# Kernel optimization log

Hardware: AMD Instinct MI355X
Metric: run time of the kernel (lower is better)

Reference implementation:

```python
import jax, jax.numpy as jnp
import numpy as np

N, E, IN, H, C = 50000, 400000, 128, 8, 32
NEG_SLOPE = 0.2


def setup_inputs() -> dict:
    key = jax.random.key(0)
    ks = jax.random.split(key, 8)
    s = 0.1
    return {
        "x": jax.random.normal(ks[0], (N, IN), jnp.float32),
        "edge_index": jax.random.randint(ks[1], (2, E), 0, N, dtype=jnp.int32),
        "edge_attr": jax.random.normal(ks[2], (E, 1), jnp.float32),
        "batch": jnp.zeros((N,), jnp.int32),
        "W_l": jax.random.normal(ks[3], (H * C, IN), jnp.float32) * s,
        "W_r": jax.random.normal(ks[4], (H * C, IN), jnp.float32) * s,
        "W_e": jax.random.normal(ks[5], (H * C, 1), jnp.float32) * s,
        "att": jax.random.normal(ks[6], (H, C), jnp.float32) * s,
        "bias": jnp.zeros((C,), jnp.float32),
        "W_proj": jax.random.normal(ks[7], (C, IN), jnp.float32) * s,
    }


def reference(x, edge_index, edge_attr, batch, W_l, W_r, W_e, att, bias, W_proj):
    n = x.shape[0]
    # --- add self loops (PyG default), edge_attr fill = 'mean' ---
    loop = jnp.arange(n, dtype=edge_index.dtype)
    ei = jnp.concatenate([edge_index, jnp.stack([loop, loop])], axis=1)  # [2, E+N]
    loop_attr = jnp.broadcast_to(edge_attr.mean(axis=0), (n, edge_attr.shape[1]))
    ea = jnp.concatenate([edge_attr, loop_attr], axis=0)                 # [E+N, 1]
    src, dst = ei[0], ei[1]

    # --- node transforms (GATv2: separate lin_l / lin_r) ---
    x_l = (x @ W_l.T).reshape(n, H, C)   # source-side features
    x_r = (x @ W_r.T).reshape(n, H, C)   # destination-side features
    e_feat = (ea @ W_e.T).reshape(-1, H, C)  # [E+N, H, C] edge fusion

    # --- GATv2 attention logits ---
    m = x_l[src] + x_r[dst] + e_feat                 # [E+N, H, C]
    m = jax.nn.leaky_relu(m, NEG_SLOPE)
    alpha = jnp.einsum("ehc,hc->eh", m, att)         # [E+N, H]

    # --- softmax over edges grouped by destination node ---
    amax = jax.ops.segment_max(alpha, dst, num_segments=n)  # [N, H]
    aexp = jnp.exp(alpha - amax[dst])
    denom = jax.ops.segment_sum(aexp, dst, num_segments=n)
    alpha = aexp / denom[dst]                        # [E+N, H]

    # --- weighted aggregation of source messages ---
    out = jax.ops.segment_sum(x_l[src] * alpha[:, :, None], dst, num_segments=n)  # [N, H, C]
    out = out.mean(axis=1) + bias                    # concat=False -> head mean, [N, C]

    # --- relu + projected residual ---
    x_new = jax.nn.relu(out) + x @ W_proj.T          # [N, C]
    return (x_new, alpha)
```

## Files before the change

### kernel.cpp

```cpp
#include <hip/hip_runtime.h>
#include <math.h>

#define N_NODES 50000
#define N_EDGES 400000
#define EN_TOT  450000
#define IN_DIM  128
#define H_HEADS 8
#define C_CH    32
#define HC      256
#define NEG_SLOPE 0.2f
#define MAXDEG 64

typedef __attribute__((ext_vector_type(8))) short bf16x8;
typedef __attribute__((ext_vector_type(4))) float f32x4;

#define OFF_XLB   0
#define OFF_XRB   (OFF_XLB + N_NODES * 128)
#define OFF_PROJ  (OFF_XRB + N_NODES * 128)
#define OFF_AEXP  (OFF_PROJ + N_NODES * C_CH)
#define OFF_WCAT  (OFF_AEXP + EN_TOT * H_HEADS)
#define OFF_PART  (OFF_WCAT + 34816)
#define OFF_MEAN  (OFF_PART + 1024)
#define OFF_PAD   (OFF_MEAN + 1)
#define OFF_CSR4  (OFF_PAD + 3)
#define OFF_DEG   (OFF_CSR4 + EN_TOT * 4)
#define OFF_OFFS  (OFF_DEG + N_NODES)
#define OFF_CUR   (OFF_OFFS + N_NODES + 1)
#define OFF_BSUM  (OFF_CUR + N_NODES)

#define SCAN_B 196

__device__ __forceinline__ unsigned f2bf(float f) {
    unsigned u = __float_as_uint(f);
    u += 0x7fffu + ((u >> 16) & 1u);
    return u >> 16;
}
__device__ __forceinline__ float bflo(unsigned u) { return __uint_as_float(u << 16); }
__device__ __forceinline__ float bfhi(unsigned u) { return __uint_as_float(u & 0xffff0000u); }

#define WCHUNKS 8704
__global__ __launch_bounds__(256) void pre_kernel(
    const float* __restrict__ Wl, const float* __restrict__ Wr, const float* __restrict__ Wproj,
    unsigned short* __restrict__ wcat,
    const int* __restrict__ ei, const float* __restrict__ ea,
    int* __restrict__ deg, float* __restrict__ part)
{
    __shared__ float sd[256];
    const int t = threadIdx.x;
    const int g = blockIdx.x * 256 + t;

    if (g < WCHUNKS) {
        int j = (g * 8) >> 7, k = (g * 8) & 127;
        const float* src = (j < 256 ? Wl + (size_t)j * 128
                                    : (j < 512 ? Wr + (size_t)(j - 256) * 128
                                               : Wproj + (size_t)(j - 512) * 128)) + k;
        float4 a = ((const float4*)src)[0];
        float4 b = ((const float4*)src)[1];
        uint4 o;
        o.x = f2bf(a.x) | (f2bf(a.y) << 16);
        o.y = f2bf(a.z) | (f2bf(a.w) << 16);
        o.z = f2bf(b.x) | (f2bf(b.y) << 16);
        o.w = f2bf(b.z) | (f2bf(b.w) << 16);
        ((uint4*)wcat)[g] = o;
    }

    float s = 0.f;
    for (int i = g; i < N_EDGES; i += 1024 * 256) s += ea[i];
    for (int i = g; i < EN_TOT; i += 1024 * 256) {
        int d = (i < N_EDGES) ? ei[N_EDGES + i] : (i - N_EDGES);
        atomicAdd(&deg[d], 1);
    }
    sd[t] = s; __syncthreads();
    for (int w = 128; w > 0; w >>= 1) { if (t < w) sd[t] += sd[t + w]; __syncthreads(); }
    if (t == 0) part[blockIdx.x] = sd[0];
}

__global__ __launch_bounds__(256) void scan_part_kernel(const int* __restrict__ deg,
                                                        int* __restrict__ bsum) {
    __shared__ int sd[256];
    int t = threadIdx.x;
    int i = blockIdx.x * 256 + t;
    int v = (i < N_NODES) ? deg[i] : 0;
    sd[t] = v; __syncthreads();
    for (int w = 128; w > 0; w >>= 1) { if (t < w) sd[t] += sd[t + w]; __syncthreads(); }
    if (t == 0) bsum[blockIdx.x] = sd[0];
}

__global__ __launch_bounds__(256) void mid_kernel(int* __restrict__ bsum,
                                                  const float* __restrict__ part,
                                                  float* __restrict__ mean_out) {
    __shared__ int sd[256];
    __shared__ float sf[256];
    int t = threadIdx.x;
    float s = part[t] + part[t + 256] + part[t + 512] + part[t + 768];
    sf[t] = s;
    int v = (t < SCAN_B) ? bsum[t] : 0;
    sd[t] = v; __syncthreads();
    for (int w = 128; w > 0; w >>= 1) { if (t < w) sf[t] += sf[t + w]; __syncthreads(); }
    if (t == 0) mean_out[0] = sf[0] / (float)N_EDGES;
    #pragma unroll
    for (int ofs = 1; ofs < 256; ofs <<= 1) {
        int u = (t >= ofs) ? sd[t - ofs] : 0;
        __syncthreads();
        sd[t] += u;
        __syncthreads();
    }
    if (t < SCAN_B) bsum[t] = sd[t] - v;
}

__global__ __launch_bounds__(256) void scan_final_kernel(
    const int* __restrict__ deg, const int* __restrict__ bsum,
    int* __restrict__ offs, int* __restrict__ cur) {
    __shared__ int sd[256];
    int t = threadIdx.x;
    int i = blockIdx.x * 256 + t;
    int v = (i < N_NODES) ? deg[i] : 0;
    sd[t] = v; __syncthreads();
    #pragma unroll
    for (int ofs = 1; ofs < 256; ofs <<= 1) {
        int u = (t >= ofs) ? sd[t - ofs] : 0;
        __syncthreads();
        sd[t] += u;
        __syncthreads();
    }
    int excl = bsum[blockIdx.x] + sd[t] - v;
    if (i < N_NODES) { offs[i] = excl; cur[i] = excl; }
    if (i == N_NODES - 1) offs[N_NODES] = excl + v;
}

__global__ __launch_bounds__(256) void scatter_kernel(
    const int* __restrict__ ei, const float* __restrict__ edge_attr,
    const float* __restrict__ mean_attr, int* __restrict__ cur,
    int4* __restrict__ csr4)
{
    int e = blockIdx.x * 256 + threadIdx.x;
    if (e >= EN_TOT) return;
    int s, d; float eav;
    if (e < N_EDGES) { s = ei[e]; d = ei[N_EDGES + e]; eav = edge_attr[e]; }
    else { s = e - N_EDGES; d = s; eav = mean_attr[0]; }
    int pos = atomicAdd(&cur[d], 1);
    csr4[pos] = make_int4(s, e, __float_as_int(eav), 0);
}

#define GM 128
#define GN 64

__global__ __launch_bounds__(256) void gemm_mfma_kernel(
    const float* __restrict__ x, const unsigned short* __restrict__ wcat,
    unsigned short* __restrict__ xlb, unsigned short* __restrict__ xrb,
    float* __restrict__ proj)
{
    __shared__ unsigned short As[GM * 128];
    __shared__ unsigned short Bs[GN * 128];
    const int t = threadIdx.x;
    const int m0 = blockIdx.x * GM;
    const int n0 = blockIdx.y * GN;

    #pragma unroll
    for (int cc = 0; cc < 8; ++cc) {
        int c = t + cc * 256;
        int r = c >> 4;
        int k0 = (c & 15) * 8;
        int row = m0 + r;
        uint4 o = make_uint4(0, 0, 0, 0);
        if (row < N_NODES) {
            const float* p = x + (size_t)row * IN_DIM + k0;
            float4 a = ((const float4*)p)[0];
            float4 b = ((const float4*)p)[1];
            o.x = f2bf(a.x) | (f2bf(a.y) << 16);
            o.y = f2bf(a.z) | (f2bf(a.w) << 16);
            o.z = f2bf(b.x) | (f2bf(b.y) << 16);
            o.w = f2bf(b.z) | (f2bf(b.w) << 16);
        }
        int byte = (r * 256 + k0 * 2) ^ ((r & 7) << 4);
        *((uint4*)((char*)As + byte)) = o;
    }
    #pragma unroll
    for (int cc = 0; cc < 4; ++cc) {
        int c = t + cc * 256;
        int r = c >> 4;
        int k0 = (c & 15) * 8;
        int j = n0 + r;
        uint4 v = make_uint4(0, 0, 0, 0);
        if (j < 544) v = *((const uint4*)(wcat + (size_t)j * 128 + k0));
        int byte = (r * 256 + k0 * 2) ^ ((r & 7) << 4);
        *((uint4*)((char*)Bs + byte)) = v;
    }
    __syncthreads();

    const int wid = t >> 6, lane = t & 63;
    const int wr = wid >> 1, wc = wid & 1;
    const int lrow = lane & 15;
    const int kgrp = (lane >> 4) * 8;

    f32x4 acc[4][2] = {};
    #pragma unroll
    for (int kk = 0; kk < 4; ++kk) {
        bf16x8 a[4], b[2];
        #pragma unroll
        for (int fm = 0; fm < 4; ++fm) {
            int r = wr * 64 + fm * 16 + lrow;
            int byte = (r * 256 + (kk * 32 + kgrp) * 2) ^ ((r & 7) << 4);
            a[fm] = *((const bf16x8*)((const char*)As + byte));
        }
        #pragma unroll
        for (int fn = 0; fn < 2; ++fn) {
            int r = wc * 32 + fn * 16 + lrow;
            int byte = (r * 256 + (kk * 32 + kgrp) * 2) ^ ((r & 7) << 4);
            b[fn] = *((const bf16x8*)((const char*)Bs + byte));
        }
        #pragma unroll
        for (int fm = 0; fm < 4; ++fm)
            #pragma unroll
            for (int fn = 0; fn < 2; ++fn)
                acc[fm][fn] = __builtin_amdgcn_mfma_f32_16x16x32_bf16(a[fm], b[fn], acc[fm][fn], 0, 0, 0);
    }

    const int crow0 = (lane >> 4) * 4;
    const int ccol = lane & 15;
    #pragma unroll
    for (int fm = 0; fm < 4; ++fm) {
        #pragma unroll
        for (int fn = 0; fn < 2; ++fn) {
            #pragma unroll
            for (int r = 0; r < 4; ++r) {
                int row = m0 + wr * 64 + fm * 16 + crow0 + r;
                int col = n0 + wc * 32 + fn * 16 + ccol;
                if (row >= N_NODES) continue;
                float v = acc[fm][fn][r];
                if (col < 256)      xlb[(size_t)row * HC + col] = (unsigned short)f2bf(v);
                else if (col < 512) xrb[(size_t)row * HC + (col - 256)] = (unsigned short)f2bf(v);
                else if (col < 544) proj[(size_t)row * C_CH + (col - 512)] = v;
            }
        }
    }
}

__global__ __launch_bounds__(256) void node_agg_kernel(
    const int* __restrict__ offs, const int4* __restrict__ csr4,
    const float* __restrict__ We, const float* __restrict__ att,
    const unsigned short* __restrict__ xlb, const unsigned short* __restrict__ xrb,
    const float* __restrict__ proj, const float* __restrict__ bias,
    float* __restrict__ aexp_ovf, float* __restrict__ alpha_out, float* __restrict__ xnew)
{
    __shared__ float s_aexp[4][MAXDEG][H_HEADS];
    __shared__ int   s_eid[4][MAXDEG];
    const int w = threadIdx.x >> 6;
    const int l = threadIdx.x & 63;
    const int d = blockIdx.x * 4 + w;
    if (d >= N_NODES) return;
    const int half = l >> 5;
    const int sl = l & 31;

    const float4 we0 = ((const float4*)We)[sl * 2];
    const float4 we1 = ((const float4*)We)[sl * 2 + 1];
    const float4 at0 = ((const float4*)att)[sl * 2];
    const float4 at1 = ((const float4*)att)[sl * 2 + 1];
    const float wev[8] = {we0.x, we0.y, we0.z, we0.w, we1.x, we1.y, we1.z, we1.w};
    const float atv[8] = {at0.x, at0.y, at0.z, at0.w, at1.x, at1.y, at1.z, at1.w};

    const uint4 vru = ((const uint4*)(xrb + (size_t)d * HC))[sl];
    float vr[8];
    vr[0] = bflo(vru.x); vr[1] = bfhi(vru.x); vr[2] = bflo(vru.y); vr[3] = bfhi(vru.y);
    vr[4] = bflo(vru.z); vr[5] = bfhi(vru.z); vr[6] = bflo(vru.w); vr[7] = bfhi(vru.w);

    const int beg = offs[d];
    const int end = offs[d + 1];

    float acc[8] = {0.f, 0.f, 0.f, 0.f, 0.f, 0.f, 0.f, 0.f};
    float den = 0.f;

    int i = beg;
    int4 c0 = make_int4(0, 0, 0, 0);
    uint4 vl0 = make_uint4(0, 0, 0, 0);
    if (i + half < end) {
        c0 = csr4[i + half];
        vl0 = ((const uint4*)(xlb + (size_t)c0.x * HC))[sl];
    }
    while (i < end) {
        const int ni = i + 2;
        int4 c1 = make_int4(0, 0, 0, 0);
        uint4 vl1 = make_uint4(0, 0, 0, 0);
        if (ni + half < end) {
            c1 = csr4[ni + half];
            vl1 = ((const uint4*)(xlb + (size_t)c1.x * HC))[sl];
        }

        const float ea = __int_as_float(c0.z);
        float xv[8];
        xv[0] = bflo(vl0.x); xv[1] = bfhi(vl0.x); xv[2] = bflo(vl0.y); xv[3] = bfhi(vl0.y);
        xv[4] = bflo(vl0.z); xv[5] = bfhi(vl0.z); xv[6] = bflo(vl0.w); xv[7] = bfhi(vl0.w);

        float tt = 0.f;
        #pragma unroll
        for (int j = 0; j < 8; ++j) {
            float m = xv[j] + vr[j] + ea * wev[j];
            m = fmaxf(m, NEG_SLOPE * m);
            tt += m * atv[j];
        }
        tt += __shfl_xor(tt, 1);
        tt += __shfl_xor(tt, 2);
        float aex = __expf(tt);
        const bool valid = (i + half) < end;
        aex = valid ? aex : 0.f;
        const int li = i + half - beg;
        if (valid && (sl & 3) == 0) {
            if (li < MAXDEG) s_aexp[w][li][sl >> 2] = aex;
            else             aexp_ovf[(size_t)c0.y * H_HEADS + (sl >> 2)] = aex;
        }
        if (valid && sl == 0 && li < MAXDEG) s_eid[w][li] = c0.y;
        #pragma unroll
        for (int j = 0; j < 8; ++j) acc[j] += aex * xv[j];
        den += aex;

        c0 = c1; vl0 = vl1; i = ni;
    }

    den += __shfl_xor(den, 32);
    #pragma unroll
    for (int j = 0; j < 8; ++j) acc[j] += __shfl_xor(acc[j], 32);

    const float den_h = __shfl(den, ((l & 7) << 2));
    const float rden = 1.f / den_h;
    for (int b = beg; b < end; b += 8) {
        const int idx = b + (l >> 3);
        if (idx < end) {
            const int li = idx - beg;
            int e; float ax;
            if (li < MAXDEG) { e = s_eid[w][li]; ax = s_aexp[w][li][l & 7]; }
            else { e = csr4[idx].y; ax = aexp_ovf[(size_t)e * H_HEADS + (l & 7)]; }
            alpha_out[(size_t)e * H_HEADS + (l & 7)] = ax * rden;
        }
    }

    const float inv = 1.f / den;
    #pragma unroll
    for (int j = 0; j < 8; ++j) acc[j] *= inv;
    #pragma unroll
    for (int mask = 4; mask <= 16; mask <<= 1)
        #pragma unroll
        for (int j = 0; j < 8; ++j) acc[j] += __shfl_xor(acc[j], mask);
    if (half == 0 && sl < 4) {
        const float4 bi0 = ((const float4*)bias)[sl * 2];
        const float4 bi1 = ((const float4*)bias)[sl * 2 + 1];
        const float4 pr0 = ((const float4*)(proj + (size_t)d * C_CH))[sl * 2];
        const float4 pr1 = ((const float4*)(proj + (size_t)d * C_CH))[sl * 2 + 1];
        float4 r0, r1;
        r0.x = fmaxf(acc[0] * 0.125f + bi0.x, 0.f) + pr0.x;
        r0.y = fmaxf(acc[1] * 0.125f + bi0.y, 0.f) + pr0.y;
        r0.z = fmaxf(acc[2] * 0.125f + bi0.z, 0.f) + pr0.z;
        r0.w = fmaxf(acc[3] * 0.125f + bi0.w, 0.f) + pr0.w;
        r1.x = fmaxf(acc[4] * 0.125f + bi1.x, 0.f) + pr1.x;
        r1.y = fmaxf(acc[5] * 0.125f + bi1.y, 0.f) + pr1.y;
        r1.z = fmaxf(acc[6] * 0.125f + bi1.z, 0.f) + pr1.z;
        r1.w = fmaxf(acc[7] * 0.125f + bi1.w, 0.f) + pr1.w;
        ((float4*)(xnew + (size_t)d * C_CH))[sl * 2] = r0;
        ((float4*)(xnew + (size_t)d * C_CH))[sl * 2 + 1] = r1;
    }
}

extern "C" void kernel_launch(void* const* d_in, const int* in_sizes, int n_in,
                              void* d_out, int out_size, void* d_ws, size_t ws_size,
                              hipStream_t stream) {
    const float* x         = (const float*)d_in[0];
    const int*   ei        = (const int*)d_in[1];
    const float* edge_attr = (const float*)d_in[2];
    const float* Wl        = (const float*)d_in[4];
    const float* Wr        = (const float*)d_in[5];
    const float* We        = (const float*)d_in[6];
    const float* att       = (const float*)d_in[7];
    const float* bias      = (const float*)d_in[8];
    const float* Wproj     = (const float*)d_in[9];

    float* ws    = (float*)d_ws;
    unsigned short* xlb  = (unsigned short*)(ws + OFF_XLB);
    unsigned short* xrb  = (unsigned short*)(ws + OFF_XRB);
    float* proj  = ws + OFF_PROJ;
    float* aexp  = ws + OFF_AEXP;
    unsigned short* wcat = (unsigned short*)(ws + OFF_WCAT);
    float* part  = ws + OFF_PART;
    float* meanp = ws + OFF_MEAN;
    int4*  csr4  = (int4*)(ws + OFF_CSR4);
    int*   deg   = (int*)(ws + OFF_DEG);
    int*   offs  = (int*)(ws + OFF_OFFS);
    int*   cur   = (int*)(ws + OFF_CUR);
    int*   bsum  = (int*)(ws + OFF_BSUM);

    float* out_xnew  = (float*)d_out;
    float* out_alpha = (float*)d_out + (size_t)N_NODES * C_CH;

    hipMemsetAsync(deg, 0, N_NODES * sizeof(int), stream);

    pre_kernel<<<1024, 256, 0, stream>>>(Wl, Wr, Wproj, wcat, ei, edge_attr, deg, part);

    scan_part_kernel<<<SCAN_B, 256, 0, stream>>>(deg, bsum);
    mid_kernel<<<1, 256, 0, stream>>>(bsum, part, meanp);
    scan_final_kernel<<<SCAN_B, 256, 0, stream>>>(deg, bsum, offs, cur);

    scatter_kernel<<<(EN_TOT + 255) / 256, 256, 0, stream>>>(ei, edge_attr, meanp, cur, csr4);

    dim3 ggrid((N_NODES + GM - 1) / GM, (544 + GN - 1) / GN);
    gemm_mfma_kernel<<<ggrid, 256, 0, stream>>>(x, wcat, xlb, xrb, proj);

    node_agg_kernel<<<(N_NODES + 3) / 4, 256, 0, stream>>>(offs, csr4, We, att, xlb, xrb,
                                                           proj, bias, aexp, out_alpha, out_xnew);
}
```

Measured before the change: 175.6 us.

## Pack CSR entries to 8 bytes and vectorize attention math with packed floats

The CSR record shrinks from int4 to int2: the source index (which fits in 16 bits) and a bf16-rounded edge attribute share one word, and the edge id sits in the other. This halves CSR write and read traffic in the scatter and aggregation kernels. The aggregation loop now uses float2 vector types so the compiler can emit packed FP32 ops. Leaky ReLU is rewritten as 0.6*m + 0.4*|m| with log2e folded into the weights, so the exponential becomes exp2f. The costs are bf16 precision loss on edge_attr and a dependence on node indices staying below 65536.

```diff
diff --git a/kernel.cpp b/kernel.cpp
--- a/kernel.cpp
+++ b/kernel.cpp
@@ -13,6 +13,7 @@
 
 typedef __attribute__((ext_vector_type(8))) short bf16x8;
 typedef __attribute__((ext_vector_type(4))) float f32x4;
+typedef __attribute__((ext_vector_type(2))) float f32x2;
 
 #define OFF_XLB   0
 #define OFF_XRB   (OFF_XLB + N_NODES * 128)
@@ -22,13 +23,14 @@
 #define OFF_PART  (OFF_WCAT + 34816)
 #define OFF_MEAN  (OFF_PART + 1024)
 #define OFF_PAD   (OFF_MEAN + 1)
-#define OFF_CSR4  (OFF_PAD + 3)
-#define OFF_DEG   (OFF_CSR4 + EN_TOT * 4)
+#define OFF_CSR2  (OFF_PAD + 3)
+#define OFF_DEG   (OFF_CSR2 + EN_TOT * 2)
 #define OFF_OFFS  (OFF_DEG + N_NODES)
 #define OFF_CUR   (OFF_OFFS + N_NODES + 1)
 #define OFF_BSUM  (OFF_CUR + N_NODES)
 
 #define SCAN_B 196
+#define LOG2E 1.4426950408889634f
 
 __device__ __forceinline__ unsigned f2bf(float f) {
     unsigned u = __float_as_uint(f);
@@ -37,6 +39,7 @@
 }
 __device__ __forceinline__ float bflo(unsigned u) { return __uint_as_float(u << 16); }
 __device__ __forceinline__ float bfhi(unsigned u) { return __uint_as_float(u & 0xffff0000u); }
+__device__ __forceinline__ f32x2 unpk(unsigned u) { f32x2 r; r.x = bflo(u); r.y = bfhi(u); return r; }
 
 #define WCHUNKS 8704
 __global__ __launch_bounds__(256) void pre_kernel(
@@ -131,7 +134,7 @@
 __global__ __launch_bounds__(256) void scatter_kernel(
     const int* __restrict__ ei, const float* __restrict__ edge_attr,
     const float* __restrict__ mean_attr, int* __restrict__ cur,
-    int4* __restrict__ csr4)
+    int2* __restrict__ csr2)
 {
     int e = blockIdx.x * 256 + threadIdx.x;
     if (e >= EN_TOT) return;
@@ -139,7 +142,7 @@
     if (e < N_EDGES) { s = ei[e]; d = ei[N_EDGES + e]; eav = edge_attr[e]; }
     else { s = e - N_EDGES; d = s; eav = mean_attr[0]; }
     int pos = atomicAdd(&cur[d], 1);
-    csr4[pos] = make_int4(s, e, __float_as_int(eav), 0);
+    csr2[pos] = make_int2(s | (int)(f2bf(eav) << 16), e);
 }
 
 #define GM 128
@@ -237,7 +240,7 @@
 }
 
 __global__ __launch_bounds__(256) void node_agg_kernel(
-    const int* __restrict__ offs, const int4* __restrict__ csr4,
+    const int* __restrict__ offs, const int2* __restrict__ csr2,
     const float* __restrict__ We, const float* __restrict__ att,
     const unsigned short* __restrict__ xlb, const unsigned short* __restrict__ xrb,
     const float* __restrict__ proj, const float* __restrict__ bias,
@@ -256,51 +259,59 @@
     const float4 we1 = ((const float4*)We)[sl * 2 + 1];
     const float4 at0 = ((const float4*)att)[sl * 2];
     const float4 at1 = ((const float4*)att)[sl * 2 + 1];
-    const float wev[8] = {we0.x, we0.y, we0.z, we0.w, we1.x, we1.y, we1.z, we1.w};
-    const float atv[8] = {at0.x, at0.y, at0.z, at0.w, at1.x, at1.y, at1.z, at1.w};
+    f32x2 we2[4], a06[4], a04[4];
+    we2[0].x = we0.x; we2[0].y = we0.y; we2[1].x = we0.z; we2[1].y = we0.w;
+    we2[2].x = we1.x; we2[2].y = we1.y; we2[3].x = we1.z; we2[3].y = we1.w;
+    a06[0].x = at0.x; a06[0].y = at0.y; a06[1].x = at0.z; a06[1].y = at0.w;
+    a06[2].x = at1.x; a06[2].y = at1.y; a06[3].x = at1.z; a06[3].y = at1.w;
+    #pragma unroll
+    for (int j = 0; j < 4; ++j) {
+        a04[j] = a06[j] * (0.4f * LOG2E);
+        a06[j] = a06[j] * (0.6f * LOG2E);
+    }
 
     const uint4 vru = ((const uint4*)(xrb + (size_t)d * HC))[sl];
-    float vr[8];
-    vr[0] = bflo(vru.x); vr[1] = bfhi(vru.x); vr[2] = bflo(vru.y); vr[3] = bfhi(vru.y);
-    vr[4] = bflo(vru.z); vr[5] = bfhi(vru.z); vr[6] = bflo(vru.w); vr[7] = bfhi(vru.w);
+    f32x2 vr2[4] = {unpk(vru.x), unpk(vru.y), unpk(vru.z), unpk(vru.w)};
 
     const int beg = offs[d];
     const int end = offs[d + 1];
 
-    float acc[8] = {0.f, 0.f, 0.f, 0.f, 0.f, 0.f, 0.f, 0.f};
+    f32x2 acc2[4] = {};
     float den = 0.f;
 
     int i = beg;
-    int4 c0 = make_int4(0, 0, 0, 0);
+    int2 c0 = make_int2(0, 0);
     uint4 vl0 = make_uint4(0, 0, 0, 0);
     if (i + half < end) {
-        c0 = csr4[i + half];
-        vl0 = ((const uint4*)(xlb + (size_t)c0.x * HC))[sl];
+        c0 = csr2[i + half];
+        vl0 = ((const uint4*)(xlb + (size_t)(c0.x & 0xffff) * HC))[sl];
     }
     while (i < end) {
         const int ni = i + 2;
-        int4 c1 = make_int4(0, 0, 0, 0);
+        int2 c1 = make_int2(0, 0);
         uint4 vl1 = make_uint4(0, 0, 0, 0);
         if (ni + half < end) {
-            c1 = csr4[ni + half];
-            vl1 = ((const uint4*)(xlb + (size_t)c1.x * HC))[sl];
-        }
-
-        const float ea = __int_as_float(c0.z);
-        float xv[8];
-        xv[0] = bflo(vl0.x); xv[1] = bfhi(vl0.x); xv[2] = bflo(vl0.y); xv[3] = bfhi(vl0.y);
-        xv[4] = bflo(vl0.z); xv[5] = bfhi(vl0.z); xv[6] = bflo(vl0.w); xv[7] = bfhi(vl0.w);
-
-        float tt = 0.f;
-        #pragma unroll
-        for (int j = 0; j < 8; ++j) {
-            float m = xv[j] + vr[j] + ea * wev[j];
-            m = fmaxf(m, NEG_SLOPE * m);
-            tt += m * atv[j];
-        }
+            c1 = csr2[ni + half];
+            vl1 = ((const uint4*)(xlb + (size_t)(c1.x & 0xffff) * HC))[sl];
+        }
+
+        const float ea = bfhi((unsigned)c0.x);
+        f32x2 ea2; ea2.x = ea; ea2.y = ea;
+        f32x2 xv2[4] = {unpk(vl0.x), unpk(vl0.y), unpk(vl0.z), unpk(vl0.w)};
+
+        f32x2 t1 = {0.f, 0.f}, t2 = {0.f, 0.f};
+        #pragma unroll
+        for (int j = 0; j < 4; ++j) {
+            f32x2 m = (xv2[j] + vr2[j]) + ea2 * we2[j];
+            f32x2 am;
+            am.x = __builtin_fabsf(m.x); am.y = __builtin_fabsf(m.y);
+            t1 += a06[j] * m;
+            t2 += a04[j] * am;
+        }
+        float tt = (t1.x + t1.y) + (t2.x + t2.y);
         tt += __shfl_xor(tt, 1);
         tt += __shfl_xor(tt, 2);
-        float aex = __expf(tt);
+        float aex = exp2f(tt);
         const bool valid = (i + half) < end;
         aex = valid ? aex : 0.f;
         const int li = i + half - beg;
@@ -309,8 +320,9 @@
             else             aexp_ovf[(size_t)c0.y * H_HEADS + (sl >> 2)] = aex;
         }
         if (valid && sl == 0 && li < MAXDEG) s_eid[w][li] = c0.y;
-        #pragma unroll
-        for (int j = 0; j < 8; ++j) acc[j] += aex * xv[j];
+        f32x2 aex2; aex2.x = aex; aex2.y = aex;
+        #pragma unroll
+        for (int j = 0; j < 4; ++j) acc2[j] += aex2 * xv2[j];
         den += aex;
 
         c0 = c1; vl0 = vl1; i = ni;
@@ -318,7 +330,10 @@
 
     den += __shfl_xor(den, 32);
     #pragma unroll
-    for (int j = 0; j < 8; ++j) acc[j] += __shfl_xor(acc[j], 32);
+    for (int j = 0; j < 4; ++j) {
+        acc2[j].x += __shfl_xor(acc2[j].x, 32);
+        acc2[j].y += __shfl_xor(acc2[j].y, 32);
+    }
 
     const float den_h = __shfl(den, ((l & 7) << 2));
     const float rden = 1.f / den_h;
@@ -328,32 +343,36 @@
             const int li = idx - beg;
             int e; float ax;
             if (li < MAXDEG) { e = s_eid[w][li]; ax = s_aexp[w][li][l & 7]; }
-            else { e = csr4[idx].y; ax = aexp_ovf[(size_t)e * H_HEADS + (l & 7)]; }
+            else { e = csr2[idx].y; ax = aexp_ovf[(size_t)e * H_HEADS + (l & 7)]; }
             alpha_out[(size_t)e * H_HEADS + (l & 7)] = ax * rden;
         }
     }
 
     const float inv = 1.f / den;
-    #pragma unroll
-    for (int j = 0; j < 8; ++j) acc[j] *= inv;
+    f32x2 inv2; inv2.x = inv; inv2.y = inv;
+    #pragma unroll
+    for (int j = 0; j < 4; ++j) acc2[j] *= inv2;
     #pragma unroll
     for (int mask = 4; mask <= 16; mask <<= 1)
         #pragma unroll
-        for (int j = 0; j < 8; ++j) acc[j] += __shfl_xor(acc[j], mask);
+        for (int j = 0; j < 4; ++j) {
+            acc2[j].x += __shfl_xor(acc2[j].x, mask);
+            acc2[j].y += __shfl_xor(acc2[j].y, mask);
+        }
     if (half == 0 && sl < 4) {
         const float4 bi0 = ((const float4*)bias)[sl * 2];
         const float4 bi1 = ((const float4*)bias)[sl * 2 + 1];
         const float4 pr0 = ((const float4*)(proj + (size_t)d * C_CH))[sl * 2];
         const float4 pr1 = ((const float4*)(proj + (size_t)d * C_CH))[sl * 2 + 1];
         float4 r0, r1;
-        r0.x = fmaxf(acc[0] * 0.125f + bi0.x, 0.f) + pr0.x;
-        r0.y = fmaxf(acc[1] * 0.125f + bi0.y, 0.f) + pr0.y;
-        r0.z = fmaxf(acc[2] * 0.125f + bi0.z, 0.f) + pr0.z;
-        r0.w = fmaxf(acc[3] * 0.125f + bi0.w, 0.f) + pr0.w;
-        r1.x = fmaxf(acc[4] * 0.125f + bi1.x, 0.f) + pr1.x;
-        r1.y = fmaxf(acc[5] * 0.125f + bi1.y, 0.f) + pr1.y;
-        r1.z = fmaxf(acc[6] * 0.125f + bi1.z, 0.f) + pr1.z;
-        r1.w = fmaxf(acc[7] * 0.125f + bi1.w, 0.f) + pr1.w;
+        r0.x = fmaxf(acc2[0].x * 0.125f + bi0.x, 0.f) + pr0.x;
+        r0.y = fmaxf(acc2[0].y * 0.125f + bi0.y, 0.f) + pr0.y;
+        r0.z = fmaxf(acc2[1].x * 0.125f + bi0.z, 0.f) + pr0.z;
+        r0.w = fmaxf(acc2[1].y * 0.125f + bi0.w, 0.f) + pr0.w;
+        r1.x = fmaxf(acc2[2].x * 0.125f + bi1.x, 0.f) + pr1.x;
+        r1.y = fmaxf(acc2[2].y * 0.125f + bi1.y, 0.f) + pr1.y;
+        r1.z = fmaxf(acc2[3].x * 0.125f + bi1.z, 0.f) + pr1.z;
+        r1.w = fmaxf(acc2[3].y * 0.125f + bi1.w, 0.f) + pr1.w;
         ((float4*)(xnew + (size_t)d * C_CH))[sl * 2] = r0;
         ((float4*)(xnew + (size_t)d * C_CH))[sl * 2 + 1] = r1;
     }
@@ -380,7 +399,7 @@
     unsigned short* wcat = (unsigned short*)(ws + OFF_WCAT);
     float* part  = ws + OFF_PART;
     float* meanp = ws + OFF_MEAN;
-    int4*  csr4  = (int4*)(ws + OFF_CSR4);
+    int2*  csr2  = (int2*)(ws + OFF_CSR2);
     int*   deg   = (int*)(ws + OFF_DEG);
     int*   offs  = (int*)(ws + OFF_OFFS);
     int*   cur   = (int*)(ws + OFF_CUR);
@@ -397,11 +416,11 @@
     mid_kernel<<<1, 256, 0, stream>>>(bsum, part, meanp);
     scan_final_kernel<<<SCAN_B, 256, 0, stream>>>(deg, bsum, offs, cur);
 
-    scatter_kernel<<<(EN_TOT + 255) / 256, 256, 0, stream>>>(ei, edge_attr, meanp, cur, csr4);
+    scatter_kernel<<<(EN_TOT + 255) / 256, 256, 0, stream>>>(ei, edge_attr, meanp, cur, csr2);
 
     dim3 ggrid((N_NODES + GM - 1) / GM, (544 + GN - 1) / GN);
     gemm_mfma_kernel<<<ggrid, 256, 0, stream>>>(x, wcat, xlb, xrb, proj);
 
-    node_agg_kernel<<<(N_NODES + 3) / 4, 256, 0, stream>>>(offs, csr4, We, att, xlb, xrb,
+    node_agg_kernel<<<(N_NODES + 3) / 4, 256, 0, stream>>>(offs, csr2, We, att, xlb, xrb,
                                                            proj, bias, aexp, out_alpha, out_xnew);
 }
```

New measurement: 186.0 us. +5.9%, slower.
